# Kernel optimization log

Measured on AMD Instinct MI355X. Metric: run time of the kernel, lower is better.

## Reference

```python
import jax, jax.numpy as jnp
import numpy as np

B, T, C, H = 2, 2048, 1024, 16
HD = C // H  # head dim = 64


def setup_inputs() -> dict:
    key = jax.random.key(0)
    ks = jax.random.split(key, 5)
    s = 0.02
    return {
        "x": jax.random.normal(ks[0], (B, T, C), dtype=jnp.float32),
        "w_attn": jax.random.normal(ks[1], (C, 3 * C), dtype=jnp.float32) * s,
        "b_attn": jnp.zeros((3 * C,), dtype=jnp.float32),
        "w_proj": jax.random.normal(ks[2], (C, C), dtype=jnp.float32) * s,
        "b_proj": jnp.zeros((C,), dtype=jnp.float32),
    }


def reference(x, w_attn, b_attn, w_proj, b_proj):
    Bc, Tc, Cc = x.shape
    qkv = x @ w_attn + b_attn                      # [B,T,3C]
    q, k, v = jnp.split(qkv, 3, axis=2)            # each [B,T,C]
    # [B,T,C] -> [B,H,T,HD]
    def heads(t):
        return t.reshape(Bc, Tc, H, HD).transpose(0, 2, 1, 3)
    q, k, v = heads(q), heads(k), heads(v)
    scale = 1.0 / jnp.sqrt(jnp.asarray(HD, dtype=x.dtype))
    att = jnp.einsum("bhqd,bhkd->bhqk", q, k) * scale   # [B,H,T,T]
    causal = jnp.tril(jnp.ones((Tc, Tc), dtype=bool))
    att = jnp.where(causal, att, jnp.asarray(-jnp.inf, dtype=att.dtype))
    att = jax.nn.softmax(att, axis=-1)
    y = jnp.einsum("bhqk,bhkd->bhqd", att, v)            # [B,H,T,HD]
    y = y.transpose(0, 2, 1, 3).reshape(Bc, Tc, Cc)      # [B,T,C]
    return y @ w_proj + b_proj
```

## Files before the change

kernel.cpp:

```cpp
#include <hip/hip_runtime.h>
#include <stdint.h>


typedef short bf16x8 __attribute__((ext_vector_type(8)));
typedef float f32x4 __attribute__((ext_vector_type(4)));

__device__ inline unsigned short f2bf(float f) {
  union { float f; uint32_t u; } v; v.f = f;
  uint32_t u = v.u;
  u += 0x7FFFu + ((u >> 16) & 1u);
  return (unsigned short)(u >> 16);
}

__device__ inline unsigned pkbf(float a, float b) {
  unsigned r;
  asm("v_cvt_pk_bf16_f32 %0, %1, %2" : "=v"(r) : "v"(a), "v"(b));
  return r;
}

__device__ inline float exp2_fast(float x) {
#if __has_builtin(__builtin_amdgcn_exp2f)
  return __builtin_amdgcn_exp2f(x);
#else
  float r; asm("v_exp_f32 %0, %1" : "=v"(r) : "v"(x)); return r;
#endif
}

__device__ inline void load_lds16(const unsigned short* g, unsigned short* l) {
  __builtin_amdgcn_global_load_lds(
      (const __attribute__((address_space(1))) unsigned int*)(const void*)g,
      (__attribute__((address_space(3))) unsigned int*)(void*)l, 16, 0, 0);
}

__global__ __launch_bounds__(256) void prep_kernel(
    const float* __restrict__ x, const float* __restrict__ w_attn,
    const float* __restrict__ w_proj,
    unsigned short* __restrict__ xb, unsigned short* __restrict__ wattnT,
    unsigned short* __restrict__ wprojT) {
  __shared__ float tile[32][33];
  const int b = blockIdx.x, t = threadIdx.x;
  if (b < 4096) {
    int i = b * 256 + t;
    float4 f = reinterpret_cast<const float4*>(x)[i];
    ushort4 o;
    o.x = f2bf(f.x); o.y = f2bf(f.y); o.z = f2bf(f.z); o.w = f2bf(f.w);
    reinterpret_cast<ushort4*>(xb)[i] = o;
    return;
  }
  const float* in; unsigned short* out; int R, Cn, bx, by;
  if (b < 7168) {
    int bb = b - 4096;
    in = w_attn; out = wattnT; R = 1024; Cn = 3072;
    bx = (bb % 96) * 32; by = (bb / 96) * 32;
  } else {
    int bb = b - 7168;
    in = w_proj; out = wprojT; R = 1024; Cn = 1024;
    bx = (bb % 32) * 32; by = (bb / 32) * 32;
  }
  const int tx = t & 31, ty = t >> 5;
  #pragma unroll
  for (int i = 0; i < 32; i += 8)
    tile[ty + i][tx] = in[(size_t)(by + ty + i) * Cn + bx + tx];
  __syncthreads();
  #pragma unroll
  for (int i = 0; i < 32; i += 8)
    out[(size_t)(bx + ty + i) * R + by + tx] = f2bf(tile[tx][ty + i]);
}

template<int BM, int BN>
__global__ __launch_bounds__(256) void gemm_bt_kernel(
    const unsigned short* __restrict__ A,
    const unsigned short* __restrict__ Bt,
    const float* __restrict__ bias,
    void* __restrict__ outp,
    unsigned short* __restrict__ vtp,
    int M, int N, int K, int mode) {
  constexpr int MT = BM / 32, NT = BN / 32;
  constexpr int RPWA = BM / 4, RPWB = BN / 4;
  constexpr int NJA = RPWA / 16, NJB = RPWB / 16;
  static_assert(NJA >= 1 && NJB >= 1, "need >=16 staged rows per wave");
  __shared__ unsigned short As[2][BM * 32];
  __shared__ unsigned short Bs[2][BN * 32];
  const int t = threadIdx.x;
  const int wave = t >> 6, lane = t & 63;
  const int L = lane & 15, quad = lane >> 4;
  const int wm = (wave >> 1) * (BM / 2), wn = (wave & 1) * (BN / 2);
  const int m0 = blockIdx.y * BM, n0 = blockIdx.x * BN;

  const int drow = lane >> 2;
  const int dch  = (lane & 3) ^ ((drow >> 1) & 3);
  const int foff = ((quad ^ ((L >> 1) & 3)) * 8);

  const unsigned short* Ab = A  + (size_t)(m0 + wave * RPWA + drow) * K + dch * 8;
  const unsigned short* Bb = Bt + (size_t)(n0 + wave * RPWB + drow) * K + dch * 8;

  f32x4 acc[MT][NT] = {};
  const int NK = K >> 5;

  #pragma unroll
  for (int j = 0; j < NJA; ++j)
    load_lds16(Ab + (size_t)j * 16 * K, &As[0][(wave * RPWA + j * 16) * 32]);
  #pragma unroll
  for (int j = 0; j < NJB; ++j)
    load_lds16(Bb + (size_t)j * 16 * K, &Bs[0][(wave * RPWB + j * 16) * 32]);

  int buf = 0;
  for (int kt = 0; kt < NK; ++kt) {
    asm volatile("" ::: "memory");
    __builtin_amdgcn_s_waitcnt(0x0F70);
    __builtin_amdgcn_s_barrier();
    asm volatile("" ::: "memory");

    if (kt + 1 < NK) {
      #pragma unroll
      for (int j = 0; j < NJA; ++j)
        load_lds16(Ab + (size_t)j * 16 * K + (kt + 1) * 32,
                   &As[buf ^ 1][(wave * RPWA + j * 16) * 32]);
      #pragma unroll
      for (int j = 0; j < NJB; ++j)
        load_lds16(Bb + (size_t)j * 16 * K + (kt + 1) * 32,
                   &Bs[buf ^ 1][(wave * RPWB + j * 16) * 32]);
    }

    bf16x8 af[MT], bf[NT];
    #pragma unroll
    for (int mt = 0; mt < MT; ++mt)
      af[mt] = *reinterpret_cast<const bf16x8*>(&As[buf][(wm + mt * 16 + L) * 32 + foff]);
    #pragma unroll
    for (int nt = 0; nt < NT; ++nt)
      bf[nt] = *reinterpret_cast<const bf16x8*>(&Bs[buf][(wn + nt * 16 + L) * 32 + foff]);
    __builtin_amdgcn_s_setprio(1);
    #pragma unroll
    for (int mt = 0; mt < MT; ++mt)
      #pragma unroll
      for (int nt = 0; nt < NT; ++nt)
        acc[mt][nt] = __builtin_amdgcn_mfma_f32_16x16x32_bf16(af[mt], bf[nt], acc[mt][nt], 0, 0, 0);
    __builtin_amdgcn_s_setprio(0);
    buf ^= 1;
  }

  if (mode == 0) {
    float* out = (float*)outp;
    #pragma unroll
    for (int mt = 0; mt < MT; ++mt)
      #pragma unroll
      for (int nt = 0; nt < NT; ++nt) {
        int col = n0 + wn + nt * 16 + L;
        float b = bias[col];
        #pragma unroll
        for (int r = 0; r < 4; ++r) {
          int row = m0 + wm + mt * 16 + quad * 4 + r;
          out[(size_t)row * N + col] = acc[mt][nt][r] + b;
        }
      }
  } else {
    unsigned short* qkv = (unsigned short*)outp;
    #pragma unroll
    for (int mt = 0; mt < MT; ++mt)
      #pragma unroll
      for (int nt = 0; nt < NT; ++nt) {
        int col = n0 + wn + nt * 16 + L;
        int sel = col >> 10, cc = col & 1023;
        int h = cc >> 6, d = cc & 63;
        float b = bias[col];
        float sc = (sel == 0) ? 0.18033688011112042f : 1.0f;
        #pragma unroll
        for (int r = 0; r < 4; ++r) {
          int row = m0 + wm + mt * 16 + quad * 4 + r;
          int bb = row >> 11, tt = row & 2047;
          float val = (acc[mt][nt][r] + b) * sc;
          if (sel == 2) {
            vtp[((size_t)(bb * 16 + h) * 64 + d) * 2048 + tt] = f2bf(val);
          } else {
            qkv[(((size_t)sel * 32 + (size_t)(bb * 16 + h)) * 2048 + tt) * 64 + d] = f2bf(val);
          }
        }
      }
  }
}

__global__ __launch_bounds__(256) void attn_kernel(
    const unsigned short* __restrict__ qkv,
    const unsigned short* __restrict__ vt,
    unsigned short* __restrict__ y) {
  __shared__ unsigned short Ks[3][64 * 64];
  __shared__ unsigned short Vs[3][64 * 64];
  __shared__ unsigned short Ps[4][32][72];

  const int t = threadIdx.x;
  const int wave = t >> 6, lane = t & 63;
  const int L = lane & 15, quad = lane >> 4;
  const int b = blockIdx.x;
  const int bh = (b & 7) * 4 + ((b >> 3) & 3);
  const int pi = b >> 5;
  const int tA = pi, tB = 31 - pi;
  const int rowA0 = tA * 64 + wave * 16;
  const int rowB0 = tB * 64 + wave * 16;
  const int ntiles = tB + 1;

  const unsigned short* qb  = qkv + ((size_t)bh * 2048) * 64;
  const unsigned short* kb  = qkv + ((size_t)(32 + bh) * 2048) * 64;
  const unsigned short* vtb = vt + (size_t)bh * 64 * 2048;

  const int drow = lane >> 3;
  const int dch  = (lane & 7) ^ drow;
  const int fo0 = ((quad ^ (L & 7)) * 8);
  const int fo1 = (((quad + 4) ^ (L & 7)) * 8);

  bf16x8 qfA[2], qfB[2];
  #pragma unroll
  for (int h = 0; h < 2; ++h) {
    qfA[h] = *reinterpret_cast<const bf16x8*>(qb + (size_t)(rowA0 + L) * 64 + h * 32 + quad * 8);
    qfB[h] = *reinterpret_cast<const bf16x8*>(qb + (size_t)(rowB0 + L) * 64 + h * 32 + quad * 8);
  }

  f32x4 oA[4] = {}, oB[4] = {};
  float rsA = 0.f, rsB = 0.f;

  {
    #pragma unroll
    for (int j = 0; j < 2; ++j) {
      int r0 = wave * 16 + j * 8;
      load_lds16(kb  + (size_t)(0 + r0 + drow) * 64 + dch * 8, &Ks[0][r0 * 64]);
      load_lds16(vtb + (size_t)(r0 + drow) * 2048 + 0 + dch * 8, &Vs[0][r0 * 64]);
    }
  }

  int buf = 0;
  for (int kt = 0; kt < ntiles; ++kt) {
    const int nkt = (kt + 1 < ntiles) ? kt + 1 : ntiles - 1;
    const int nbuf = (buf == 2) ? 0 : buf + 1;
    {
      const int kg = nkt * 64;
      #pragma unroll
      for (int j = 0; j < 2; ++j) {
        int r0 = wave * 16 + j * 8;
        load_lds16(kb  + (size_t)(kg + r0 + drow) * 64 + dch * 8, &Ks[nbuf][r0 * 64]);
        load_lds16(vtb + (size_t)(r0 + drow) * 2048 + kg + dch * 8, &Vs[nbuf][r0 * 64]);
      }
    }
    asm volatile("" ::: "memory");
    __builtin_amdgcn_s_waitcnt(0x0F74);
    __builtin_amdgcn_s_barrier();
    asm volatile("" ::: "memory");

    const bool actA = (kt <= tA);

    bf16x8 kf[4][2];
    #pragma unroll
    for (int nt = 0; nt < 4; ++nt) {
      kf[nt][0] = *reinterpret_cast<const bf16x8*>(&Ks[buf][(nt * 16 + L) * 64 + fo0]);
      kf[nt][1] = *reinterpret_cast<const bf16x8*>(&Ks[buf][(nt * 16 + L) * 64 + fo1]);
    }

    f32x4 sB[4] = {};
    __builtin_amdgcn_s_setprio(1);
    #pragma unroll
    for (int nt = 0; nt < 4; ++nt) {
      sB[nt] = __builtin_amdgcn_mfma_f32_16x16x32_bf16(kf[nt][0], qfB[0], sB[nt], 0, 0, 0);
      sB[nt] = __builtin_amdgcn_mfma_f32_16x16x32_bf16(kf[nt][1], qfB[1], sB[nt], 0, 0, 0);
    }
    __builtin_amdgcn_s_setprio(0);
    if (kt == tB) {
      #pragma unroll
      for (int nt = 0; nt < 4; ++nt) {
        int key0 = kt * 64 + nt * 16 + quad * 4;
        int qr = rowB0 + L;
        #pragma unroll
        for (int r = 0; r < 4; ++r)
          if (key0 + r > qr) sB[nt][r] = -3.0e38f;
      }
    }
    #pragma unroll
    for (int nt = 0; nt < 4; ++nt) {
      float p0 = exp2_fast(sB[nt][0]), p1 = exp2_fast(sB[nt][1]);
      float p2 = exp2_fast(sB[nt][2]), p3 = exp2_fast(sB[nt][3]);
      rsB += (p0 + p1) + (p2 + p3);
      uint2 pk;
      pk.x = pkbf(p0, p1);
      pk.y = pkbf(p2, p3);
      *reinterpret_cast<uint2*>(&Ps[wave][16 + L][nt * 16 + quad * 4]) = pk;
    }

    if (actA) {
      f32x4 sA[4] = {};
      __builtin_amdgcn_s_setprio(1);
      #pragma unroll
      for (int nt = 0; nt < 4; ++nt) {
        sA[nt] = __builtin_amdgcn_mfma_f32_16x16x32_bf16(kf[nt][0], qfA[0], sA[nt], 0, 0, 0);
        sA[nt] = __builtin_amdgcn_mfma_f32_16x16x32_bf16(kf[nt][1], qfA[1], sA[nt], 0, 0, 0);
      }
      __builtin_amdgcn_s_setprio(0);
      if (kt == tA) {
        #pragma unroll
        for (int nt = 0; nt < 4; ++nt) {
          int key0 = kt * 64 + nt * 16 + quad * 4;
          int qr = rowA0 + L;
          #pragma unroll
          for (int r = 0; r < 4; ++r)
            if (key0 + r > qr) sA[nt][r] = -3.0e38f;
        }
      }
      #pragma unroll
      for (int nt = 0; nt < 4; ++nt) {
        float p0 = exp2_fast(sA[nt][0]), p1 = exp2_fast(sA[nt][1]);
        float p2 = exp2_fast(sA[nt][2]), p3 = exp2_fast(sA[nt][3]);
        rsA += (p0 + p1) + (p2 + p3);
        uint2 pk;
        pk.x = pkbf(p0, p1);
        pk.y = pkbf(p2, p3);
        *reinterpret_cast<uint2*>(&Ps[wave][L][nt * 16 + quad * 4]) = pk;
      }
    }

    bf16x8 vf[4][2];
    #pragma unroll
    for (int nt = 0; nt < 4; ++nt) {
      vf[nt][0] = *reinterpret_cast<const bf16x8*>(&Vs[buf][(nt * 16 + L) * 64 + fo0]);
      vf[nt][1] = *reinterpret_cast<const bf16x8*>(&Vs[buf][(nt * 16 + L) * 64 + fo1]);
    }
    bf16x8 pb0 = *reinterpret_cast<const bf16x8*>(&Ps[wave][16 + L][quad * 8]);
    bf16x8 pb1 = *reinterpret_cast<const bf16x8*>(&Ps[wave][16 + L][32 + quad * 8]);
    __builtin_amdgcn_s_setprio(1);
    #pragma unroll
    for (int nt = 0; nt < 4; ++nt) {
      oB[nt] = __builtin_amdgcn_mfma_f32_16x16x32_bf16(pb0, vf[nt][0], oB[nt], 0, 0, 0);
      oB[nt] = __builtin_amdgcn_mfma_f32_16x16x32_bf16(pb1, vf[nt][1], oB[nt], 0, 0, 0);
    }
    __builtin_amdgcn_s_setprio(0);
    if (actA) {
      bf16x8 pa0 = *reinterpret_cast<const bf16x8*>(&Ps[wave][L][quad * 8]);
      bf16x8 pa1 = *reinterpret_cast<const bf16x8*>(&Ps[wave][L][32 + quad * 8]);
      __builtin_amdgcn_s_setprio(1);
      #pragma unroll
      for (int nt = 0; nt < 4; ++nt) {
        oA[nt] = __builtin_amdgcn_mfma_f32_16x16x32_bf16(pa0, vf[nt][0], oA[nt], 0, 0, 0);
        oA[nt] = __builtin_amdgcn_mfma_f32_16x16x32_bf16(pa1, vf[nt][1], oA[nt], 0, 0, 0);
      }
      __builtin_amdgcn_s_setprio(0);
    }
    buf = nbuf;
  }

  float a = rsA; a += __shfl_xor(a, 16, 64); a += __shfl_xor(a, 32, 64);
  float b2 = rsB; b2 += __shfl_xor(b2, 16, 64); b2 += __shfl_xor(b2, 32, 64);
  float invA[4], invB[4];
  #pragma unroll
  for (int r = 0; r < 4; ++r) {
    invA[r] = 1.0f / __shfl(a, quad * 4 + r, 64);
    invB[r] = 1.0f / __shfl(b2, quad * 4 + r, 64);
  }
  const int bb = bh >> 4, hh = bh & 15;
  #pragma unroll
  for (int nt = 0; nt < 4; ++nt)
    #pragma unroll
    for (int r = 0; r < 4; ++r) {
      int rA = rowA0 + quad * 4 + r;
      int rB = rowB0 + quad * 4 + r;
      int col = hh * 64 + nt * 16 + L;
      y[((size_t)bb * 2048 + rA) * 1024 + col] = f2bf(oA[nt][r] * invA[r]);
      y[((size_t)bb * 2048 + rB) * 1024 + col] = f2bf(oB[nt][r] * invB[r]);
    }
  __builtin_amdgcn_s_waitcnt(0);
}

extern "C" void kernel_launch(void* const* d_in, const int* in_sizes, int n_in,
                              void* d_out, int out_size, void* d_ws, size_t ws_size,
                              hipStream_t stream) {
  const float* x      = (const float*)d_in[0];
  const float* w_attn = (const float*)d_in[1];
  const float* b_attn = (const float*)d_in[2];
  const float* w_proj = (const float*)d_in[3];
  const float* b_proj = (const float*)d_in[4];
  float* out = (float*)d_out;

  unsigned short* ws = (unsigned short*)d_ws;
  unsigned short* xb     = ws;
  unsigned short* wattnT = xb + 4194304;
  unsigned short* wprojT = wattnT + 3145728;
  unsigned short* qkv    = wprojT + 1048576;
  unsigned short* yb     = qkv + 12582912;
  unsigned short* vt     = yb + 4194304;

  prep_kernel<<<8192, 256, 0, stream>>>(x, w_attn, w_proj, xb, wattnT, wprojT);

  gemm_bt_kernel<128, 192><<<dim3(16, 32), 256, 0, stream>>>(xb, wattnT, b_attn, qkv, vt, 4096, 3072, 1024, 1);
  attn_kernel<<<dim3(512), 256, 0, stream>>>(qkv, vt, yb);
  gemm_bt_kernel<64, 64><<<dim3(16, 64), 256, 0, stream>>>(yb, wprojT, b_proj, out, nullptr, 4096, 1024, 1024, 0);
}
```

Measured before the change: 209.7 us.

## Add dedicated 256x192 QKV GEMM kernel with 512 threads and BK=64

Replaces the generic templated GEMM for the QKV projection with a specialized kernel using 256x192 block tiles, 8 waves, a K-step of 64 with XOR-swizzled LDS layout, and finer-grained barrier-interleaved MFMA phases. The larger tile raises arithmetic intensity per LDS load, and the wider K step halves loop iterations. The cost is a grid of only 256 blocks with much larger LDS use (about 112KB double-buffered), which limits occupancy and may underfill the 256 CUs. The generic GEMM is simplified to the fp32-output mode only.

```diff
diff --git a/kernel.cpp b/kernel.cpp
--- a/kernel.cpp
+++ b/kernel.cpp
@@ -67,18 +67,121 @@
     out[(size_t)(bx + ty + i) * R + by + tx] = f2bf(tile[tx][ty + i]);
 }
 
+__global__ __launch_bounds__(512) void gemm_qkv_kernel(
+    const unsigned short* __restrict__ A,
+    const unsigned short* __restrict__ Bt,
+    const float* __restrict__ bias,
+    unsigned short* __restrict__ qkv,
+    unsigned short* __restrict__ vtp) {
+  constexpr int K = 1024;
+  __shared__ unsigned short As[2][256 * 64];
+  __shared__ unsigned short Bs[2][192 * 64];
+  const int t = threadIdx.x;
+  const int wave = t >> 6, lane = t & 63;
+  const int L = lane & 15, quad = lane >> 4;
+  const int wm = (wave >> 2) * 128, wn = (wave & 3) * 48;
+  const int m0 = blockIdx.y * 256, n0 = blockIdx.x * 192;
+
+  const int drow = lane >> 3;
+  const int dch  = (lane & 7) ^ drow;
+  const int fo0 = ((quad ^ (L & 7)) * 8);
+  const int fo1 = (((quad + 4) ^ (L & 7)) * 8);
+
+  const unsigned short* Ab = A  + (size_t)(m0 + wave * 32 + drow) * K + dch * 8;
+  const unsigned short* Bb = Bt + (size_t)(n0 + wave * 24 + drow) * K + dch * 8;
+
+  f32x4 acc[8][3] = {};
+
+  #pragma unroll
+  for (int j = 0; j < 4; ++j)
+    load_lds16(Ab + (size_t)j * 8 * K, &As[0][(wave * 32 + j * 8) * 64]);
+  #pragma unroll
+  for (int j = 0; j < 3; ++j)
+    load_lds16(Bb + (size_t)j * 8 * K, &Bs[0][(wave * 24 + j * 8) * 64]);
+
+  for (int kt = 0; kt < 16; ++kt) {
+    const int cur = kt & 1;
+    asm volatile("" ::: "memory");
+    __builtin_amdgcn_s_waitcnt(0x0F70);
+    __builtin_amdgcn_s_barrier();
+    asm volatile("" ::: "memory");
+
+    bf16x8 bf[2][3];
+    #pragma unroll
+    for (int p = 0; p < 4; ++p) {
+      if (p == 0) {
+        if (kt + 1 < 16) {
+          #pragma unroll
+          for (int j = 0; j < 4; ++j)
+            load_lds16(Ab + (size_t)j * 8 * K + (size_t)(kt + 1) * 64,
+                       &As[cur ^ 1][(wave * 32 + j * 8) * 64]);
+          #pragma unroll
+          for (int j = 0; j < 3; ++j)
+            load_lds16(Bb + (size_t)j * 8 * K + (size_t)(kt + 1) * 64,
+                       &Bs[cur ^ 1][(wave * 24 + j * 8) * 64]);
+        }
+        #pragma unroll
+        for (int nt = 0; nt < 3; ++nt) {
+          bf[0][nt] = *reinterpret_cast<const bf16x8*>(&Bs[cur][(wn + nt * 16 + L) * 64 + fo0]);
+          bf[1][nt] = *reinterpret_cast<const bf16x8*>(&Bs[cur][(wn + nt * 16 + L) * 64 + fo1]);
+        }
+      }
+      bf16x8 af[2][2];
+      #pragma unroll
+      for (int h = 0; h < 2; ++h) {
+        const int mt = 2 * p + h;
+        af[h][0] = *reinterpret_cast<const bf16x8*>(&As[cur][(wm + mt * 16 + L) * 64 + fo0]);
+        af[h][1] = *reinterpret_cast<const bf16x8*>(&As[cur][(wm + mt * 16 + L) * 64 + fo1]);
+      }
+      asm volatile("" ::: "memory");
+      __builtin_amdgcn_s_barrier();
+      __builtin_amdgcn_s_setprio(1);
+      #pragma unroll
+      for (int h = 0; h < 2; ++h)
+        #pragma unroll
+        for (int nt = 0; nt < 3; ++nt) {
+          acc[2 * p + h][nt] = __builtin_amdgcn_mfma_f32_16x16x32_bf16(af[h][0], bf[0][nt], acc[2 * p + h][nt], 0, 0, 0);
+          acc[2 * p + h][nt] = __builtin_amdgcn_mfma_f32_16x16x32_bf16(af[h][1], bf[1][nt], acc[2 * p + h][nt], 0, 0, 0);
+        }
+      __builtin_amdgcn_s_setprio(0);
+      asm volatile("" ::: "memory");
+      __builtin_amdgcn_s_barrier();
+    }
+  }
+
+  #pragma unroll
+  for (int mt = 0; mt < 8; ++mt)
+    #pragma unroll
+    for (int nt = 0; nt < 3; ++nt) {
+      int col = n0 + wn + nt * 16 + L;
+      int sel = col >> 10, cc = col & 1023;
+      int h = cc >> 6, d = cc & 63;
+      float b = bias[col];
+      float sc = (sel == 0) ? 0.18033688011112042f : 1.0f;
+      #pragma unroll
+      for (int r = 0; r < 4; ++r) {
+        int row = m0 + wm + mt * 16 + quad * 4 + r;
+        int bb = row >> 11, tt = row & 2047;
+        float val = (acc[mt][nt][r] + b) * sc;
+        if (sel == 2) {
+          vtp[((size_t)(bb * 16 + h) * 64 + d) * 2048 + tt] = f2bf(val);
+        } else {
+          qkv[(((size_t)sel * 32 + (size_t)(bb * 16 + h)) * 2048 + tt) * 64 + d] = f2bf(val);
+        }
+      }
+    }
+}
+
 template<int BM, int BN>
 __global__ __launch_bounds__(256) void gemm_bt_kernel(
     const unsigned short* __restrict__ A,
     const unsigned short* __restrict__ Bt,
     const float* __restrict__ bias,
-    void* __restrict__ outp,
-    unsigned short* __restrict__ vtp,
-    int M, int N, int K, int mode) {
+    float* __restrict__ out,
+    int M, int N, int K) {
   constexpr int MT = BM / 32, NT = BN / 32;
   constexpr int RPWA = BM / 4, RPWB = BN / 4;
   constexpr int NJA = RPWA / 16, NJB = RPWB / 16;
-  static_assert(NJA >= 1 && NJB >= 1, "need >=16 staged rows per wave");
   __shared__ unsigned short As[2][BM * 32];
   __shared__ unsigned short Bs[2][BN * 32];
   const int t = threadIdx.x;
@@ -139,44 +242,18 @@
     buf ^= 1;
   }
 
-  if (mode == 0) {
-    float* out = (float*)outp;
-    #pragma unroll
-    for (int mt = 0; mt < MT; ++mt)
-      #pragma unroll
-      for (int nt = 0; nt < NT; ++nt) {
-        int col = n0 + wn + nt * 16 + L;
-        float b = bias[col];
-        #pragma unroll
-        for (int r = 0; r < 4; ++r) {
-          int row = m0 + wm + mt * 16 + quad * 4 + r;
-          out[(size_t)row * N + col] = acc[mt][nt][r] + b;
-        }
-      }
-  } else {
-    unsigned short* qkv = (unsigned short*)outp;
-    #pragma unroll
-    for (int mt = 0; mt < MT; ++mt)
-      #pragma unroll
-      for (int nt = 0; nt < NT; ++nt) {
-        int col = n0 + wn + nt * 16 + L;
-        int sel = col >> 10, cc = col & 1023;
-        int h = cc >> 6, d = cc & 63;
-        float b = bias[col];
-        float sc = (sel == 0) ? 0.18033688011112042f : 1.0f;
-        #pragma unroll
-        for (int r = 0; r < 4; ++r) {
-          int row = m0 + wm + mt * 16 + quad * 4 + r;
-          int bb = row >> 11, tt = row & 2047;
-          float val = (acc[mt][nt][r] + b) * sc;
-          if (sel == 2) {
-            vtp[((size_t)(bb * 16 + h) * 64 + d) * 2048 + tt] = f2bf(val);
-          } else {
-            qkv[(((size_t)sel * 32 + (size_t)(bb * 16 + h)) * 2048 + tt) * 64 + d] = f2bf(val);
-          }
-        }
-      }
-  }
+  #pragma unroll
+  for (int mt = 0; mt < MT; ++mt)
+    #pragma unroll
+    for (int nt = 0; nt < NT; ++nt) {
+      int col = n0 + wn + nt * 16 + L;
+      float b = bias[col];
+      #pragma unroll
+      for (int r = 0; r < 4; ++r) {
+        int row = m0 + wm + mt * 16 + quad * 4 + r;
+        out[(size_t)row * N + col] = acc[mt][nt][r] + b;
+      }
+    }
 }
 
 __global__ __launch_bounds__(256) void attn_kernel(
@@ -384,7 +461,7 @@
 
   prep_kernel<<<8192, 256, 0, stream>>>(x, w_attn, w_proj, xb, wattnT, wprojT);
 
-  gemm_bt_kernel<128, 192><<<dim3(16, 32), 256, 0, stream>>>(xb, wattnT, b_attn, qkv, vt, 4096, 3072, 1024, 1);
+  gemm_qkv_kernel<<<dim3(16, 16), 512, 0, stream>>>(xb, wattnT, b_attn, qkv, vt);
   attn_kernel<<<dim3(512), 256, 0, stream>>>(qkv, vt, yb);
-  gemm_bt_kernel<64, 64><<<dim3(16, 64), 256, 0, stream>>>(yb, wprojT, b_proj, out, nullptr, 4096, 1024, 1024, 0);
-}
+  gemm_bt_kernel<64, 64><<<dim3(16, 64), 256, 0, stream>>>(yb, wprojT, b_proj, out, 4096, 1024, 1024);
+}
```

Measured after the change: 192.5 us. 1.09x faster.
